# Performance work log

Hardware: AMD Instinct MI355X
Metric: run time of the kernel (lower is better)

The kernel has to match this reference:

```python
import jax, jax.numpy as jnp
import numpy as np

NUM_NODES = 15000


def _gcn_conv(x, W, b, src, dst, norm, num_nodes):
    # PyG GCNConv: x' = D^-1/2 (A + I) D^-1/2 (x W) + b
    h = x @ W                                   # [N, out]
    msg = h[src] * norm[:, None]                # gather + scale per edge
    out = jax.ops.segment_sum(msg, dst, num_segments=num_nodes)
    return out + b


def setup_inputs() -> dict:
    key = jax.random.key(0)
    ks = jax.random.split(key, 12)
    T = 100000
    E = 200000
    inp = {
        "x": jax.random.normal(ks[0], (NUM_NODES, 768), jnp.float32),
        "r_emb": jax.random.normal(ks[1], (T, 768), jnp.float32),
        "W1": jax.random.normal(ks[2], (768, 10), jnp.float32) * 0.05,
        "b1": jax.random.normal(ks[3], (10,), jnp.float32) * 0.05,
        "W2": jax.random.normal(ks[4], (10, 128), jnp.float32) * 0.05,
        "b2": jax.random.normal(ks[5], (128,), jnp.float32) * 0.05,
        "W_ih": jax.random.normal(ks[6], (512, 1024), jnp.float32) * 0.03,
        "W_hh": jax.random.normal(ks[7], (512, 128), jnp.float32) * 0.03,
        "b_ih": jax.random.normal(ks[8], (512,), jnp.float32) * 0.03,
        "b_hh": jax.random.normal(ks[9], (512,), jnp.float32) * 0.03,
        "edge_index": jax.random.randint(ks[10], (2, E), 0, NUM_NODES).astype(jnp.int64),
        "triples": jax.random.randint(ks[11], (T, 3), 0, NUM_NODES).astype(jnp.int64),
    }
    return inp


def reference(x, r_emb, W1, b1, W2, b2, W_ih, W_hh, b_ih, b_hh, edge_index, triples):
    N = x.shape[0]
    H = 128  # lstm hidden size
    # --- add self loops, symmetric GCN normalization ---
    loop = jnp.arange(N, dtype=edge_index.dtype)
    src = jnp.concatenate([edge_index[0], loop])
    dst = jnp.concatenate([edge_index[1], loop])
    deg = jax.ops.segment_sum(jnp.ones_like(dst, jnp.float32), dst, num_segments=N)
    dinv = jnp.where(deg > 0, jax.lax.rsqrt(deg), 0.0)
    norm = dinv[src] * dinv[dst]                      # [E+N]
    # --- 2-layer GCN ---
    h = jax.nn.relu(_gcn_conv(x, W1, b1, src, dst, norm, N))   # [N, 10]
    z = _gcn_conv(h, W2, b2, src, dst, norm, N)                # [N, 128]
    # --- per-triple LSTM scoring, batched (seq_len=1, zero init state) ---
    hvec = z[triples[:, 0]]                           # [T, 128]
    tvec = z[triples[:, 2]]                           # [T, 128]
    feat = jnp.concatenate([hvec, r_emb, tvec], axis=-1)       # [T, 1024]
    gates = feat @ W_ih.T + (b_ih + b_hh)             # [T, 512]; h0=0 so W_hh term vanishes
    i_g, f_g, g_g, o_g = jnp.split(gates, 4, axis=-1)  # torch gate order i,f,g,o
    c = jax.nn.sigmoid(i_g) * jnp.tanh(g_g)           # c0 = 0 -> forget term drops
    out = jax.nn.sigmoid(o_g) * jnp.tanh(c)           # [T, 128]
    score = jax.nn.sigmoid(jnp.sum(out, axis=-1))     # [T]
    return score
```

## Files before the change

### kernel.cpp

```cpp
#include <hip/hip_runtime.h>

#define NF 768
#define D1 10
#define D2 128
#define BM 64

typedef __attribute__((ext_vector_type(8))) short bf16x8;
typedef __attribute__((ext_vector_type(16))) float f32x16;

static __device__ __forceinline__ float sigf(float v){ return 1.0f/(1.0f+__expf(-v)); }
static __device__ __forceinline__ float tanhfast(float v){ return 2.0f/(1.0f+__expf(-2.0f*v)) - 1.0f; }
static __device__ __forceinline__ short f2bf(float f){
    unsigned u = __float_as_uint(f);
    u += 0x7fffu + ((u>>16)&1u);
    return (short)(u>>16);
}

static __device__ __forceinline__ void gload16(const void* g, void* l){
    __builtin_amdgcn_global_load_lds(
        (const __attribute__((address_space(1))) unsigned int*)(unsigned long long)g,
        (__attribute__((address_space(3))) unsigned int*)(unsigned long long)l,
        16, 0, 0);
}

static __device__ __forceinline__ bf16x8 cvt8(float4 a, float4 b){
    unsigned u0,u1,u2,u3;
    asm("v_cvt_pk_bf16_f32 %0, %1, %2" : "=v"(u0) : "v"(a.x), "v"(a.y));
    asm("v_cvt_pk_bf16_f32 %0, %1, %2" : "=v"(u1) : "v"(a.z), "v"(a.w));
    asm("v_cvt_pk_bf16_f32 %0, %1, %2" : "=v"(u2) : "v"(b.x), "v"(b.y));
    asm("v_cvt_pk_bf16_f32 %0, %1, %2" : "=v"(u3) : "v"(b.z), "v"(b.w));
    union { unsigned u[4]; bf16x8 v; } r;
    r.u[0]=u0; r.u[1]=u1; r.u[2]=u2; r.u[3]=u3;
    return r.v;
}

__global__ void k_deg(const int* __restrict__ dst, int* __restrict__ cnt, int E){
    int e = blockIdx.x*256 + threadIdx.x;
    if(e<E) atomicAdd(&cnt[dst[e]], 1);
}

__global__ __launch_bounds__(256) void k_scan(const int* __restrict__ cnt,
                                              int* __restrict__ rowptr, int* __restrict__ rowcur,
                                              float* __restrict__ dinv, int N, int E){
    __shared__ int part[256];
    int t = threadIdx.x;
    int C = (N+255)/256;
    int lo = t*C, hi = lo+C; if(hi>N) hi=N; if(lo>N) lo=N;
    int s=0;
    for(int i=lo;i<hi;i++) s += cnt[i];
    part[t]=s;
    __syncthreads();
    if(t==0){
        int run=0;
        for(int i=0;i<256;i++){ int v=part[i]; part[i]=run; run+=v; }
        rowptr[N]=E;
    }
    __syncthreads();
    int run = part[t];
    for(int i=lo;i<hi;i++){
        rowptr[i]=run; rowcur[i]=run; run += cnt[i];
        dinv[i] = rsqrtf((float)cnt[i] + 1.0f);
    }
}

__global__ void k_fill(const int* __restrict__ src, const int* __restrict__ dst,
                       const float* __restrict__ dinv, int* __restrict__ rowcur,
                       int* __restrict__ esrc, float* __restrict__ enorm, int E){
    int e = blockIdx.x*256 + threadIdx.x;
    if(e>=E) return;
    int s=src[e], d=dst[e];
    int pos = atomicAdd(&rowcur[d], 1);
    esrc[pos]=s;
    enorm[pos]=dinv[s]*dinv[d];
}

__global__ __launch_bounds__(256) void k_h1(const float* __restrict__ x,
                                            const float* __restrict__ W1,
                                            float* __restrict__ h1, int N){
    __shared__ float wt[D1*NF];
    for(int idx=threadIdx.x; idx<NF*D1; idx+=256){
        int k=idx/D1, c=idx-k*D1;
        wt[c*NF+k]=W1[idx];
    }
    __syncthreads();
    int row = blockIdx.x*4 + (threadIdx.x>>6);
    int lane = threadIdx.x&63;
    if(row>=N) return;
    const float4* xr = (const float4*)(x + (size_t)row*NF);
    float acc[D1];
#pragma unroll
    for(int c=0;c<D1;c++) acc[c]=0.f;
#pragma unroll
    for(int i=0;i<3;i++){
        float4 v = xr[lane + 64*i];
#pragma unroll
        for(int c=0;c<D1;c++){
            float4 w = *(const float4*)&wt[c*NF + (lane+64*i)*4];
            acc[c] += v.x*w.x + v.y*w.y + v.z*w.z + v.w*w.w;
        }
    }
#pragma unroll
    for(int c=0;c<D1;c++){
        float v=acc[c];
#pragma unroll
        for(int off=32;off;off>>=1) v += __shfl_down(v,off,64);
        acc[c]=v;
    }
    if(lane==0){
#pragma unroll
        for(int c=0;c<D1;c++) h1[(size_t)row*D1+c]=acc[c];
    }
}

__global__ __launch_bounds__(256) void k_gath1(const float* __restrict__ h1,
        const int* __restrict__ rowptr, const int* __restrict__ esrc,
        const float* __restrict__ enorm, const float* __restrict__ dinv,
        const float* __restrict__ b1, float* __restrict__ h, int N){
    int node = blockIdx.x*4 + (threadIdx.x>>6);
    int lane = threadIdx.x&63;
    if(node>=N) return;
    int e0=rowptr[node], e1=rowptr[node+1];
    float acc[D1];
#pragma unroll
    for(int c=0;c<D1;c++) acc[c]=0.f;
    for(int e=e0+lane; e<e1; e+=64){
        int s=esrc[e]; float w=enorm[e];
        const float* hr = h1 + (size_t)s*D1;
#pragma unroll
        for(int c=0;c<D1;c++) acc[c] += hr[c]*w;
    }
    if(lane==0){
        float di=dinv[node], d2=di*di;
        const float* hr = h1 + (size_t)node*D1;
#pragma unroll
        for(int c=0;c<D1;c++) acc[c] += hr[c]*d2;
    }
#pragma unroll
    for(int c=0;c<D1;c++){
        float v=acc[c];
#pragma unroll
        for(int off=32;off;off>>=1) v += __shfl_down(v,off,64);
        acc[c]=v;
    }
    if(lane==0){
#pragma unroll
        for(int c=0;c<D1;c++){
            float v = acc[c] + b1[c];
            h[(size_t)node*D1+c] = v>0.f ? v : 0.f;
        }
    }
}

__global__ __launch_bounds__(128) void k_hz(const float* __restrict__ h,
                                            const float* __restrict__ W2,
                                            float* __restrict__ hz, int N){
    __shared__ float w2s[D1*D2];
    int j = threadIdx.x;
    for(int i=j;i<D1*D2;i+=128) w2s[i]=W2[i];
    __syncthreads();
    int n = blockIdx.x;
    if(n>=N) return;
    const float* hr = h + (size_t)n*D1;
    float acc=0.f;
#pragma unroll
    for(int k=0;k<D1;k++) acc += hr[k]*w2s[k*D2+j];
    hz[(size_t)n*D2+j]=acc;
}

__global__ __launch_bounds__(128) void k_gath2(const float* __restrict__ hz,
        const int* __restrict__ rowptr, const int* __restrict__ esrc,
        const float* __restrict__ enorm, const float* __restrict__ dinv,
        const float* __restrict__ b2, float* __restrict__ zbf, int N){
    int n = blockIdx.x;
    int c = threadIdx.x;
    int e0 = rowptr[n], e1 = rowptr[n+1];
    float di = dinv[n];
    float acc = hz[(size_t)n*D2+c]*di*di + b2[c];
    int e = e0;
    for(; e+1<e1; e+=2){
        int s0=esrc[e], s1=esrc[e+1];
        float w0=enorm[e], w1=enorm[e+1];
        acc += hz[(size_t)s0*D2+c]*w0 + hz[(size_t)s1*D2+c]*w1;
    }
    if(e<e1) acc += hz[(size_t)esrc[e]*D2+c]*enorm[e];
    zbf[(size_t)n*D2+c] = acc;
}

__global__ void k_wimgB(const float* __restrict__ Wih, ushort* __restrict__ img){
    int gid = blockIdx.x*256 + threadIdx.x;
    if(gid >= 12*64*64) return;
    int l = gid & 63;
    int ks16 = (gid>>6) & 63;
    int f = gid >> 12;
    int dd = l & 31, kb = l>>5;
    int wn = f/3, gi = f - wn*3;
    int gbase = (gi==0)?0:((gi==1)?256:384);
    int wrow = gbase + wn*32 + dd;
    int k = ks16*16 + kb*8;
    const float* p = Wih + (size_t)wrow*1024 + k;
    float4 v0=*(const float4*)p, v1=*(const float4*)(p+4);
    bf16x8 o;
    o[0]=f2bf(v0.x); o[1]=f2bf(v0.y); o[2]=f2bf(v0.z); o[3]=f2bf(v0.w);
    o[4]=f2bf(v1.x); o[5]=f2bf(v1.y); o[6]=f2bf(v1.z); o[7]=f2bf(v1.w);
    *(bf16x8*)(img + (size_t)gid*8) = o;
}

__global__ __launch_bounds__(256,2) void k_big(
    const float* __restrict__ remb, const ushort* __restrict__ img,
    const float* __restrict__ zbf, const float* __restrict__ b_ih,
    const float* __restrict__ b_hh, const int* __restrict__ trip,
    float* __restrict__ score, int T)
{
    __shared__ float  Ar[4][64*32];
    __shared__ ushort Br[2][24*64*8];
    int tid=threadIdx.x, lane=tid&63, w=tid>>6;
    int l31=lane&31, lh=lane>>5;
    int t0=blockIdx.x*BM;

    const int arow = lane>>3;
    const int lsl  = ((lane&7) ^ arow)*4;
    int tcA[2], thA[2], ttA[2];
#pragma unroll
    for(int j=0;j<2;j++){
        int row = w*16 + j*8 + arow;
        int tc = t0+row; if(tc>=T) tc=T-1;
        tcA[j]=tc; thA[j]=trip[3*tc]; ttA[j]=trip[3*tc+2];
    }
    const int rx = l31&7;

    f32x16 acc[2][3];
    const f32x16 zer = {0,0,0,0,0,0,0,0,0,0,0,0,0,0,0,0};
#pragma unroll
    for(int m=0;m<2;m++)
#pragma unroll
        for(int g=0;g<3;g++) acc[m][g]=zer;

#define AISSUE(C_) if((C_)<32){ \
    _Pragma("unroll") \
    for(int j_=0;j_<2;j_++){ \
        const float* s_; \
        if((C_)<4)       s_ = zbf + (size_t)thA[j_]*D2 + (C_)*32 + lsl; \
        else if((C_)<28) s_ = remb + (size_t)tcA[j_]*NF + ((C_)-4)*32 + lsl; \
        else             s_ = zbf + (size_t)ttA[j_]*D2 + ((C_)-28)*32 + lsl; \
        gload16(s_, &Ar[(C_)&3][(w*16 + j_*8)*32]); \
    } }

#define BISSUE(C_) if((C_)<32){ \
    _Pragma("unroll") \
    for(int j_=0;j_<6;j_++){ \
        const int i_ = w*6+j_, f_ = i_>>1, s_ = i_&1; \
        gload16(img + ((size_t)(f_*64 + (C_)*2 + s_)*64 + lane)*8, \
                &Br[(C_)&1][(f_*2+s_)*64*8]); \
    } }

#define KSTEP(C_,S_) { \
    const float* ar_ = &Ar[(C_)&3][0]; \
    const ushort* br_ = &Br[(C_)&1][0]; \
    const int q0_ = (S_)*4 + lh*2; \
    float4 a00_ = *(const float4*)&ar_[ l31*32      + ((q0_  )^rx)*4 ]; \
    float4 a01_ = *(const float4*)&ar_[ l31*32      + ((q0_+1)^rx)*4 ]; \
    bf16x8 A0_ = cvt8(a00_,a01_); \
    float4 a10_ = *(const float4*)&ar_[ (32+l31)*32 + ((q0_  )^rx)*4 ]; \
    float4 a11_ = *(const float4*)&ar_[ (32+l31)*32 + ((q0_+1)^rx)*4 ]; \
    bf16x8 A1_ = cvt8(a10_,a11_); \
    bf16x8 B0_ = *(const bf16x8*)&br_[(((w*3+0)*2+(S_))*64 + lane)*8]; \
    bf16x8 B1_ = *(const bf16x8*)&br_[(((w*3+1)*2+(S_))*64 + lane)*8]; \
    bf16x8 B2_ = *(const bf16x8*)&br_[(((w*3+2)*2+(S_))*64 + lane)*8]; \
    acc[0][0]=__builtin_amdgcn_mfma_f32_32x32x16_bf16(A0_,B0_,acc[0][0],0,0,0); \
    acc[0][1]=__builtin_amdgcn_mfma_f32_32x32x16_bf16(A0_,B1_,acc[0][1],0,0,0); \
    acc[0][2]=__builtin_amdgcn_mfma_f32_32x32x16_bf16(A0_,B2_,acc[0][2],0,0,0); \
    acc[1][0]=__builtin_amdgcn_mfma_f32_32x32x16_bf16(A1_,B0_,acc[1][0],0,0,0); \
    acc[1][1]=__builtin_amdgcn_mfma_f32_32x32x16_bf16(A1_,B1_,acc[1][1],0,0,0); \
    acc[1][2]=__builtin_amdgcn_mfma_f32_32x32x16_bf16(A1_,B2_,acc[1][2],0,0,0); \
}

#define CHUNK(C_,W_) { \
    asm volatile("s_waitcnt vmcnt(" W_ ")" ::: "memory"); \
    __builtin_amdgcn_s_barrier(); \
    __builtin_amdgcn_sched_barrier(0); \
    BISSUE((C_)+1) \
    AISSUE((C_)+3) \
    __builtin_amdgcn_sched_barrier(0); \
    __builtin_amdgcn_s_setprio(1); \
    KSTEP(C_,0) KSTEP(C_,1) \
    __builtin_amdgcn_s_setprio(0); \
}

    AISSUE(0) AISSUE(1) BISSUE(0) AISSUE(2)
    __builtin_amdgcn_sched_barrier(0);

    CHUNK(0 ,"2") CHUNK(1 ,"2") CHUNK(2 ,"2") CHUNK(3 ,"2")
    CHUNK(4 ,"2") CHUNK(5 ,"2") CHUNK(6 ,"2") CHUNK(7 ,"2")
    CHUNK(8 ,"2") CHUNK(9 ,"2") CHUNK(10,"2") CHUNK(11,"2")
    CHUNK(12,"2") CHUNK(13,"2") CHUNK(14,"2") CHUNK(15,"2")
    CHUNK(16,"2") CHUNK(17,"2") CHUNK(18,"2") CHUNK(19,"2")
    CHUNK(20,"2") CHUNK(21,"2") CHUNK(22,"2") CHUNK(23,"2")
    CHUNK(24,"2") CHUNK(25,"2") CHUNK(26,"2") CHUNK(27,"2")
    CHUNK(28,"2") CHUNK(29,"2") CHUNK(30,"0") CHUNK(31,"0")
#undef CHUNK
#undef KSTEP
#undef BISSUE
#undef AISSUE

    float* rowsum = &Ar[0][0];
    __syncthreads();
    if(tid<BM) rowsum[tid]=0.f;
    __syncthreads();
    int d = w*32+l31;
    float bi=b_ih[d]+b_hh[d];
    float bg=b_ih[256+d]+b_hh[256+d];
    float bo=b_ih[384+d]+b_hh[384+d];
#pragma unroll
    for(int m=0;m<2;m++){
#pragma unroll
        for(int r=0;r<16;r++){
            int row = m*32 + (r&3)+8*(r>>2)+4*lh;
            float ig = acc[m][0][r] + bi;
            float gg = acc[m][1][r] + bg;
            float og = acc[m][2][r] + bo;
            float cc = sigf(ig)*tanhfast(gg);
            float ov = sigf(og)*tanhfast(cc);
#pragma unroll
            for(int off=1; off<32; off<<=1) ov += __shfl_xor(ov, off, 64);
            if(l31==0) atomicAdd(&rowsum[row], ov);
        }
    }
    __syncthreads();
    if(tid < BM){
        int t = t0 + tid;
        if(t < T) score[t] = sigf(rowsum[tid]);
    }
}

extern "C" void kernel_launch(void* const* d_in, const int* in_sizes, int n_in,
                              void* d_out, int out_size, void* d_ws, size_t ws_size,
                              hipStream_t stream){
    const float* x    = (const float*)d_in[0];
    const float* remb = (const float*)d_in[1];
    const float* W1   = (const float*)d_in[2];
    const float* b1   = (const float*)d_in[3];
    const float* W2   = (const float*)d_in[4];
    const float* b2   = (const float*)d_in[5];
    const float* Wih  = (const float*)d_in[6];
    const float* b_ih = (const float*)d_in[8];
    const float* b_hh = (const float*)d_in[9];
    const int*   ei   = (const int*)d_in[10];
    const int*   trip = (const int*)d_in[11];
    float* score = (float*)d_out;

    const int N = in_sizes[0]/NF;
    const int E = in_sizes[10]/2;
    const int T = in_sizes[11]/3;
    const int* src = ei;
    const int* dst = ei + E;

    float* ws = (float*)d_ws;
    size_t o = 0;
    ushort* img  = (ushort*)(ws+o); o += (size_t)12*64*64*8/2;
    float* zbf   = ws+o;            o += (size_t)N*D2;
    int*   cnt    = (int*)(ws+o);   o += (size_t)((N+8)&~7);
    int*   rowptr = (int*)(ws+o);   o += (size_t)((N+8)&~7);
    int*   rowcur = (int*)(ws+o);   o += (size_t)((N+8)&~7);
    int*   esrc   = (int*)(ws+o);   o += (size_t)E;
    float* enorm  = ws+o;           o += (size_t)E;
    float* dinv   = ws+o;           o += (size_t)((N+7)&~7);
    float* h1     = ws+o;           o += (size_t)N*D1;
    float* hbuf   = ws+o;           o += (size_t)N*D1;
    float* hz     = ws+o;           o += (size_t)N*D2;
    (void)ws_size; (void)n_in; (void)out_size;

    hipMemsetAsync(cnt, 0, (size_t)N*sizeof(int), stream);

    k_wimgB<<<dim3((12*64*64+255)/256), dim3(256), 0, stream>>>(Wih, img);
    k_deg  <<<dim3((E+255)/256), dim3(256), 0, stream>>>(dst, cnt, E);
    k_scan <<<dim3(1), dim3(256), 0, stream>>>(cnt, rowptr, rowcur, dinv, N, E);
    k_fill <<<dim3((E+255)/256), dim3(256), 0, stream>>>(src, dst, dinv, rowcur, esrc, enorm, E);
    k_h1   <<<dim3((N+3)/4), dim3(256), 0, stream>>>(x, W1, h1, N);
    k_gath1<<<dim3((N+3)/4), dim3(256), 0, stream>>>(h1, rowptr, esrc, enorm, dinv, b1, hbuf, N);
    k_hz   <<<dim3(N), dim3(128), 0, stream>>>(hbuf, W2, hz, N);
    k_gath2<<<dim3(N), dim3(128), 0, stream>>>(hz, rowptr, esrc, enorm, dinv, b2, zbf, N);
    k_big  <<<dim3((T+BM-1)/BM), dim3(256), 0, stream>>>(remb, img, zbf, b_ih, b_hh, trip, score, T);
}
```

Before: 324.5 us.

## Stage A operand as bf16 in LDS via register prefetch, triple-buffer B

The A operand (gathered z rows and r_emb) no longer goes through direct global-to-LDS copies as fp32. Each thread now loads it into registers, converts it to bf16 once, and writes a smaller swizzled bf16 tile to LDS. The K loop moves to 64 steps of 16, with B triple-buffered and a four-deep register prefetch of A, and the occupancy hint rises to 3 blocks per CU. This cuts LDS footprint and removes the redundant per-wave conversion, at the cost of more barriers per K element, more register pressure and exposure to register-load latency.

Result: faster. 302.2 us (-6.9%).

```diff
diff --git a/kernel.cpp b/kernel.cpp
--- a/kernel.cpp
+++ b/kernel.cpp
@@ -23,15 +23,13 @@
         16, 0, 0);
 }
 
-static __device__ __forceinline__ bf16x8 cvt8(float4 a, float4 b){
-    unsigned u0,u1,u2,u3;
+static __device__ __forceinline__ short4 cvt4(float4 a){
+    unsigned u0,u1;
     asm("v_cvt_pk_bf16_f32 %0, %1, %2" : "=v"(u0) : "v"(a.x), "v"(a.y));
     asm("v_cvt_pk_bf16_f32 %0, %1, %2" : "=v"(u1) : "v"(a.z), "v"(a.w));
-    asm("v_cvt_pk_bf16_f32 %0, %1, %2" : "=v"(u2) : "v"(b.x), "v"(b.y));
-    asm("v_cvt_pk_bf16_f32 %0, %1, %2" : "=v"(u3) : "v"(b.z), "v"(b.w));
-    union { unsigned u[4]; bf16x8 v; } r;
-    r.u[0]=u0; r.u[1]=u1; r.u[2]=u2; r.u[3]=u3;
-    return r.v;
+    union { unsigned u[2]; short4 s; } r;
+    r.u[0]=u0; r.u[1]=u1;
+    return r.s;
 }
 
 __global__ void k_deg(const int* __restrict__ dst, int* __restrict__ cnt, int E){
@@ -205,28 +203,28 @@
     *(bf16x8*)(img + (size_t)gid*8) = o;
 }
 
-__global__ __launch_bounds__(256,2) void k_big(
+__global__ __launch_bounds__(256,3) void k_big(
     const float* __restrict__ remb, const ushort* __restrict__ img,
     const float* __restrict__ zbf, const float* __restrict__ b_ih,
     const float* __restrict__ b_hh, const int* __restrict__ trip,
     float* __restrict__ score, int T)
 {
-    __shared__ float  Ar[4][64*32];
-    __shared__ ushort Br[2][24*64*8];
+    __shared__ ushort Ab[2][64*16];
+    __shared__ ushort Br[3][12*512];
     int tid=threadIdx.x, lane=tid&63, w=tid>>6;
     int l31=lane&31, lh=lane>>5;
     int t0=blockIdx.x*BM;
 
-    const int arow = lane>>3;
-    const int lsl  = ((lane&7) ^ arow)*4;
-    int tcA[2], thA[2], ttA[2];
-#pragma unroll
-    for(int j=0;j<2;j++){
-        int row = w*16 + j*8 + arow;
-        int tc = t0+row; if(tc>=T) tc=T-1;
-        tcA[j]=tc; thA[j]=trip[3*tc]; ttA[j]=trip[3*tc+2];
-    }
-    const int rx = l31&7;
+    const int arow = w*16 + (lane>>2);
+    const int asub = lane&3;
+    { }
+    int tc = t0 + arow; if(tc>=T) tc=T-1;
+    const float* pzh = zbf + (size_t)trip[3*tc]*D2   + asub*4;
+    const float* prm = remb + (size_t)tc*NF          + asub*4;
+    const float* pzt = zbf + (size_t)trip[3*tc+2]*D2 + asub*4;
+    const int awoff = arow*16 + (((asub>>1) ^ (arow&1))*8) + (asub&1)*4;
+    const int ar0 = (l31)*16    + ((lh ^ (l31&1))*8);
+    const int ar1 = (32+l31)*16 + ((lh ^ (l31&1))*8);
 
     f32x16 acc[2][3];
     const f32x16 zer = {0,0,0,0,0,0,0,0,0,0,0,0,0,0,0,0};
@@ -235,74 +233,75 @@
 #pragma unroll
         for(int g=0;g<3;g++) acc[m][g]=zer;
 
-#define AISSUE(C_) if((C_)<32){ \
+    float4 pa[4];
+
+#define ALOAD(C_) if((C_)<64){ \
+    const float* s_; \
+    if((C_)<8)       s_ = pzh + (C_)*16; \
+    else if((C_)<56) s_ = prm + ((C_)-8)*16; \
+    else             s_ = pzt + ((C_)-56)*16; \
+    pa[(C_)&3] = *(const float4*)s_; }
+
+#define AWRITE(C_) if((C_)<64){ \
+    *(short4*)&Ab[(C_)&1][awoff] = cvt4(pa[(C_)&3]); }
+
+#define BISSUE(C_) if((C_)<64){ \
     _Pragma("unroll") \
-    for(int j_=0;j_<2;j_++){ \
-        const float* s_; \
-        if((C_)<4)       s_ = zbf + (size_t)thA[j_]*D2 + (C_)*32 + lsl; \
-        else if((C_)<28) s_ = remb + (size_t)tcA[j_]*NF + ((C_)-4)*32 + lsl; \
-        else             s_ = zbf + (size_t)ttA[j_]*D2 + ((C_)-28)*32 + lsl; \
-        gload16(s_, &Ar[(C_)&3][(w*16 + j_*8)*32]); \
+    for(int j_=0;j_<3;j_++){ \
+        gload16(img + ((size_t)((w*3+j_)*64 + (C_))*64 + lane)*8, \
+                &Br[(C_)%3][(w*3+j_)*512]); \
     } }
 
-#define BISSUE(C_) if((C_)<32){ \
-    _Pragma("unroll") \
-    for(int j_=0;j_<6;j_++){ \
-        const int i_ = w*6+j_, f_ = i_>>1, s_ = i_&1; \
-        gload16(img + ((size_t)(f_*64 + (C_)*2 + s_)*64 + lane)*8, \
-                &Br[(C_)&1][(f_*2+s_)*64*8]); \
-    } }
-
-#define KSTEP(C_,S_) { \
-    const float* ar_ = &Ar[(C_)&3][0]; \
-    const ushort* br_ = &Br[(C_)&1][0]; \
-    const int q0_ = (S_)*4 + lh*2; \
-    float4 a00_ = *(const float4*)&ar_[ l31*32      + ((q0_  )^rx)*4 ]; \
-    float4 a01_ = *(const float4*)&ar_[ l31*32      + ((q0_+1)^rx)*4 ]; \
-    bf16x8 A0_ = cvt8(a00_,a01_); \
-    float4 a10_ = *(const float4*)&ar_[ (32+l31)*32 + ((q0_  )^rx)*4 ]; \
-    float4 a11_ = *(const float4*)&ar_[ (32+l31)*32 + ((q0_+1)^rx)*4 ]; \
-    bf16x8 A1_ = cvt8(a10_,a11_); \
-    bf16x8 B0_ = *(const bf16x8*)&br_[(((w*3+0)*2+(S_))*64 + lane)*8]; \
-    bf16x8 B1_ = *(const bf16x8*)&br_[(((w*3+1)*2+(S_))*64 + lane)*8]; \
-    bf16x8 B2_ = *(const bf16x8*)&br_[(((w*3+2)*2+(S_))*64 + lane)*8]; \
-    acc[0][0]=__builtin_amdgcn_mfma_f32_32x32x16_bf16(A0_,B0_,acc[0][0],0,0,0); \
-    acc[0][1]=__builtin_amdgcn_mfma_f32_32x32x16_bf16(A0_,B1_,acc[0][1],0,0,0); \
-    acc[0][2]=__builtin_amdgcn_mfma_f32_32x32x16_bf16(A0_,B2_,acc[0][2],0,0,0); \
-    acc[1][0]=__builtin_amdgcn_mfma_f32_32x32x16_bf16(A1_,B0_,acc[1][0],0,0,0); \
-    acc[1][1]=__builtin_amdgcn_mfma_f32_32x32x16_bf16(A1_,B1_,acc[1][1],0,0,0); \
-    acc[1][2]=__builtin_amdgcn_mfma_f32_32x32x16_bf16(A1_,B2_,acc[1][2],0,0,0); \
-}
-
-#define CHUNK(C_,W_) { \
+#define CH(C_,W_) { \
     asm volatile("s_waitcnt vmcnt(" W_ ")" ::: "memory"); \
+    __builtin_amdgcn_sched_barrier(0); \
+    asm volatile("s_waitcnt lgkmcnt(0)" ::: "memory"); \
     __builtin_amdgcn_s_barrier(); \
     __builtin_amdgcn_sched_barrier(0); \
-    BISSUE((C_)+1) \
-    AISSUE((C_)+3) \
+    BISSUE((C_)+2) \
     __builtin_amdgcn_sched_barrier(0); \
-    __builtin_amdgcn_s_setprio(1); \
-    KSTEP(C_,0) KSTEP(C_,1) \
-    __builtin_amdgcn_s_setprio(0); \
-}
-
-    AISSUE(0) AISSUE(1) BISSUE(0) AISSUE(2)
+    ALOAD((C_)+4) \
+    __builtin_amdgcn_sched_barrier(0); \
+    { \
+        const ushort* a_ = &Ab[(C_)&1][0]; \
+        const ushort* b_ = &Br[(C_)%3][0]; \
+        bf16x8 A0_ = *(const bf16x8*)&a_[ar0]; \
+        bf16x8 A1_ = *(const bf16x8*)&a_[ar1]; \
+        bf16x8 B0_ = *(const bf16x8*)&b_[((w*3+0)*64+lane)*8]; \
+        bf16x8 B1_ = *(const bf16x8*)&b_[((w*3+1)*64+lane)*8]; \
+        bf16x8 B2_ = *(const bf16x8*)&b_[((w*3+2)*64+lane)*8]; \
+        __builtin_amdgcn_s_setprio(1); \
+        acc[0][0]=__builtin_amdgcn_mfma_f32_32x32x16_bf16(A0_,B0_,acc[0][0],0,0,0); \
+        acc[0][1]=__builtin_amdgcn_mfma_f32_32x32x16_bf16(A0_,B1_,acc[0][1],0,0,0); \
+        acc[0][2]=__builtin_amdgcn_mfma_f32_32x32x16_bf16(A0_,B2_,acc[0][2],0,0,0); \
+        acc[1][0]=__builtin_amdgcn_mfma_f32_32x32x16_bf16(A1_,B0_,acc[1][0],0,0,0); \
+        acc[1][1]=__builtin_amdgcn_mfma_f32_32x32x16_bf16(A1_,B1_,acc[1][1],0,0,0); \
+        acc[1][2]=__builtin_amdgcn_mfma_f32_32x32x16_bf16(A1_,B2_,acc[1][2],0,0,0); \
+        __builtin_amdgcn_s_setprio(0); \
+    } \
+    AWRITE((C_)+1) \
+}
+
+    ALOAD(0) ALOAD(1) ALOAD(2) ALOAD(3)
     __builtin_amdgcn_sched_barrier(0);
-
-    CHUNK(0 ,"2") CHUNK(1 ,"2") CHUNK(2 ,"2") CHUNK(3 ,"2")
-    CHUNK(4 ,"2") CHUNK(5 ,"2") CHUNK(6 ,"2") CHUNK(7 ,"2")
-    CHUNK(8 ,"2") CHUNK(9 ,"2") CHUNK(10,"2") CHUNK(11,"2")
-    CHUNK(12,"2") CHUNK(13,"2") CHUNK(14,"2") CHUNK(15,"2")
-    CHUNK(16,"2") CHUNK(17,"2") CHUNK(18,"2") CHUNK(19,"2")
-    CHUNK(20,"2") CHUNK(21,"2") CHUNK(22,"2") CHUNK(23,"2")
-    CHUNK(24,"2") CHUNK(25,"2") CHUNK(26,"2") CHUNK(27,"2")
-    CHUNK(28,"2") CHUNK(29,"2") CHUNK(30,"0") CHUNK(31,"0")
-#undef CHUNK
-#undef KSTEP
+    BISSUE(0) BISSUE(1)
+    __builtin_amdgcn_sched_barrier(0);
+    AWRITE(0)
+
+    CH(0 ,"3") CH(1 ,"4") CH(2 ,"5") CH(3 ,"5") CH(4 ,"5") CH(5 ,"5") CH(6 ,"5") CH(7 ,"5")
+    CH(8 ,"5") CH(9 ,"5") CH(10,"5") CH(11,"5") CH(12,"5") CH(13,"5") CH(14,"5") CH(15,"5")
+    CH(16,"5") CH(17,"5") CH(18,"5") CH(19,"5") CH(20,"5") CH(21,"5") CH(22,"5") CH(23,"5")
+    CH(24,"5") CH(25,"5") CH(26,"5") CH(27,"5") CH(28,"5") CH(29,"5") CH(30,"5") CH(31,"5")
+    CH(32,"5") CH(33,"5") CH(34,"5") CH(35,"5") CH(36,"5") CH(37,"5") CH(38,"5") CH(39,"5")
+    CH(40,"5") CH(41,"5") CH(42,"5") CH(43,"5") CH(44,"5") CH(45,"5") CH(46,"5") CH(47,"5")
+    CH(48,"5") CH(49,"5") CH(50,"5") CH(51,"5") CH(52,"5") CH(53,"5") CH(54,"5") CH(55,"5")
+    CH(56,"5") CH(57,"5") CH(58,"5") CH(59,"5") CH(60,"5") CH(61,"4") CH(62,"3") CH(63,"0")
+#undef CH
 #undef BISSUE
-#undef AISSUE
-
-    float* rowsum = &Ar[0][0];
+#undef AWRITE
+#undef ALOAD
+
+    float* rowsum = (float*)&Br[0][0];
     __syncthreads();
     if(tid<BM) rowsum[tid]=0.f;
     __syncthreads();
```

## Replace multi-stage async LDS pipeline with single-buffered loop and raise occupancy

Applied to the files above, without the earlier changes.

Drops the 4-stage A and 2-stage B LDS ring buffers and the explicit vmcnt/sched_barrier pipeline, using one buffer per operand with two __syncthreads per k-chunk. Launch bounds go from 2 to 3 blocks per CU, relying on the smaller LDS footprint and more resident blocks to hide load latency instead of prefetching in software. The cost is exposed global-load latency inside each block and more barriers, and register pressure may be squeezed by the higher occupancy target.

After: 327.1 us. About the same (+0.8%).

```diff
diff --git a/kernel.cpp b/kernel.cpp
--- a/kernel.cpp
+++ b/kernel.cpp
@@ -205,28 +205,30 @@
     *(bf16x8*)(img + (size_t)gid*8) = o;
 }
 
-__global__ __launch_bounds__(256,2) void k_big(
+__global__ __launch_bounds__(256,3) void k_big(
     const float* __restrict__ remb, const ushort* __restrict__ img,
     const float* __restrict__ zbf, const float* __restrict__ b_ih,
     const float* __restrict__ b_hh, const int* __restrict__ trip,
     float* __restrict__ score, int T)
 {
-    __shared__ float  Ar[4][64*32];
-    __shared__ ushort Br[2][24*64*8];
+    __shared__ float  As[64*32];
+    __shared__ ushort Bs[24*64*8];
     int tid=threadIdx.x, lane=tid&63, w=tid>>6;
     int l31=lane&31, lh=lane>>5;
     int t0=blockIdx.x*BM;
 
-    const int arow = lane>>3;
-    const int lsl  = ((lane&7) ^ arow)*4;
-    int tcA[2], thA[2], ttA[2];
+    const int aoff = ((lane&7) ^ (lane>>3))*4;
+    const float* pzh[2]; const float* prm[2]; const float* pzt[2];
 #pragma unroll
     for(int j=0;j<2;j++){
-        int row = w*16 + j*8 + arow;
+        int row = w*16 + j*8 + (lane>>3);
         int tc = t0+row; if(tc>=T) tc=T-1;
-        tcA[j]=tc; thA[j]=trip[3*tc]; ttA[j]=trip[3*tc+2];
-    }
-    const int rx = l31&7;
+        pzh[j] = zbf + (size_t)trip[3*tc]*D2   + aoff;
+        prm[j] = remb + (size_t)tc*NF          + aoff;
+        pzt[j] = zbf + (size_t)trip[3*tc+2]*D2 + aoff;
+    }
+    float* adst0 = &As[(w*16+0)*32];
+    float* adst1 = &As[(w*16+8)*32];
 
     f32x16 acc[2][3];
     const f32x16 zer = {0,0,0,0,0,0,0,0,0,0,0,0,0,0,0,0};
@@ -235,75 +237,45 @@
 #pragma unroll
         for(int g=0;g<3;g++) acc[m][g]=zer;
 
-#define AISSUE(C_) if((C_)<32){ \
-    _Pragma("unroll") \
-    for(int j_=0;j_<2;j_++){ \
-        const float* s_; \
-        if((C_)<4)       s_ = zbf + (size_t)thA[j_]*D2 + (C_)*32 + lsl; \
-        else if((C_)<28) s_ = remb + (size_t)tcA[j_]*NF + ((C_)-4)*32 + lsl; \
-        else             s_ = zbf + (size_t)ttA[j_]*D2 + ((C_)-28)*32 + lsl; \
-        gload16(s_, &Ar[(C_)&3][(w*16 + j_*8)*32]); \
-    } }
-
-#define BISSUE(C_) if((C_)<32){ \
-    _Pragma("unroll") \
-    for(int j_=0;j_<6;j_++){ \
-        const int i_ = w*6+j_, f_ = i_>>1, s_ = i_&1; \
-        gload16(img + ((size_t)(f_*64 + (C_)*2 + s_)*64 + lane)*8, \
-                &Br[(C_)&1][(f_*2+s_)*64*8]); \
-    } }
-
-#define KSTEP(C_,S_) { \
-    const float* ar_ = &Ar[(C_)&3][0]; \
-    const ushort* br_ = &Br[(C_)&1][0]; \
-    const int q0_ = (S_)*4 + lh*2; \
-    float4 a00_ = *(const float4*)&ar_[ l31*32      + ((q0_  )^rx)*4 ]; \
-    float4 a01_ = *(const float4*)&ar_[ l31*32      + ((q0_+1)^rx)*4 ]; \
-    bf16x8 A0_ = cvt8(a00_,a01_); \
-    float4 a10_ = *(const float4*)&ar_[ (32+l31)*32 + ((q0_  )^rx)*4 ]; \
-    float4 a11_ = *(const float4*)&ar_[ (32+l31)*32 + ((q0_+1)^rx)*4 ]; \
-    bf16x8 A1_ = cvt8(a10_,a11_); \
-    bf16x8 B0_ = *(const bf16x8*)&br_[(((w*3+0)*2+(S_))*64 + lane)*8]; \
-    bf16x8 B1_ = *(const bf16x8*)&br_[(((w*3+1)*2+(S_))*64 + lane)*8]; \
-    bf16x8 B2_ = *(const bf16x8*)&br_[(((w*3+2)*2+(S_))*64 + lane)*8]; \
-    acc[0][0]=__builtin_amdgcn_mfma_f32_32x32x16_bf16(A0_,B0_,acc[0][0],0,0,0); \
-    acc[0][1]=__builtin_amdgcn_mfma_f32_32x32x16_bf16(A0_,B1_,acc[0][1],0,0,0); \
-    acc[0][2]=__builtin_amdgcn_mfma_f32_32x32x16_bf16(A0_,B2_,acc[0][2],0,0,0); \
-    acc[1][0]=__builtin_amdgcn_mfma_f32_32x32x16_bf16(A1_,B0_,acc[1][0],0,0,0); \
-    acc[1][1]=__builtin_amdgcn_mfma_f32_32x32x16_bf16(A1_,B1_,acc[1][1],0,0,0); \
-    acc[1][2]=__builtin_amdgcn_mfma_f32_32x32x16_bf16(A1_,B2_,acc[1][2],0,0,0); \
-}
-
-#define CHUNK(C_,W_) { \
-    asm volatile("s_waitcnt vmcnt(" W_ ")" ::: "memory"); \
-    __builtin_amdgcn_s_barrier(); \
-    __builtin_amdgcn_sched_barrier(0); \
-    BISSUE((C_)+1) \
-    AISSUE((C_)+3) \
-    __builtin_amdgcn_sched_barrier(0); \
-    __builtin_amdgcn_s_setprio(1); \
-    KSTEP(C_,0) KSTEP(C_,1) \
-    __builtin_amdgcn_s_setprio(0); \
-}
-
-    AISSUE(0) AISSUE(1) BISSUE(0) AISSUE(2)
-    __builtin_amdgcn_sched_barrier(0);
-
-    CHUNK(0 ,"2") CHUNK(1 ,"2") CHUNK(2 ,"2") CHUNK(3 ,"2")
-    CHUNK(4 ,"2") CHUNK(5 ,"2") CHUNK(6 ,"2") CHUNK(7 ,"2")
-    CHUNK(8 ,"2") CHUNK(9 ,"2") CHUNK(10,"2") CHUNK(11,"2")
-    CHUNK(12,"2") CHUNK(13,"2") CHUNK(14,"2") CHUNK(15,"2")
-    CHUNK(16,"2") CHUNK(17,"2") CHUNK(18,"2") CHUNK(19,"2")
-    CHUNK(20,"2") CHUNK(21,"2") CHUNK(22,"2") CHUNK(23,"2")
-    CHUNK(24,"2") CHUNK(25,"2") CHUNK(26,"2") CHUNK(27,"2")
-    CHUNK(28,"2") CHUNK(29,"2") CHUNK(30,"0") CHUNK(31,"0")
-#undef CHUNK
-#undef KSTEP
-#undef BISSUE
-#undef AISSUE
-
-    float* rowsum = &Ar[0][0];
-    __syncthreads();
+    const int rx7 = l31&7;
+
+    for(int s=0;s<32;s++){
+        const float *sa0, *sa1;
+        if(s<4)      { sa0=pzh[0]+s*32;      sa1=pzh[1]+s*32; }
+        else if(s<28){ sa0=prm[0]+(s-4)*32;  sa1=prm[1]+(s-4)*32; }
+        else         { sa0=pzt[0]+(s-28)*32; sa1=pzt[1]+(s-28)*32; }
+        gload16(sa0, adst0);
+        gload16(sa1, adst1);
+#pragma unroll
+        for(int j=0;j<6;j++){
+            int f = w*3 + (j>>1), sh = j&1;
+            gload16(img + ((size_t)(f*64 + s*2 + sh)*64 + lane)*8,
+                    &Bs[(size_t)((f*2+sh)*64)*8]);
+        }
+        __syncthreads();
+#pragma unroll
+        for(int h=0;h<2;h++){
+            int u0 = h*4 + lh*2;
+            float4 a00 = *(const float4*)&As[ l31*32     + ((u0  )^rx7)*4];
+            float4 a01 = *(const float4*)&As[ l31*32     + ((u0+1)^rx7)*4];
+            bf16x8 A0 = cvt8(a00,a01);
+            float4 a10 = *(const float4*)&As[(32+l31)*32 + ((u0  )^rx7)*4];
+            float4 a11 = *(const float4*)&As[(32+l31)*32 + ((u0+1)^rx7)*4];
+            bf16x8 A1 = cvt8(a10,a11);
+            bf16x8 B0 = *(const bf16x8*)&Bs[(size_t)(((w*3+0)*2+h)*64+lane)*8];
+            bf16x8 B1 = *(const bf16x8*)&Bs[(size_t)(((w*3+1)*2+h)*64+lane)*8];
+            bf16x8 B2 = *(const bf16x8*)&Bs[(size_t)(((w*3+2)*2+h)*64+lane)*8];
+            acc[0][0]=__builtin_amdgcn_mfma_f32_32x32x16_bf16(A0,B0,acc[0][0],0,0,0);
+            acc[0][1]=__builtin_amdgcn_mfma_f32_32x32x16_bf16(A0,B1,acc[0][1],0,0,0);
+            acc[0][2]=__builtin_amdgcn_mfma_f32_32x32x16_bf16(A0,B2,acc[0][2],0,0,0);
+            acc[1][0]=__builtin_amdgcn_mfma_f32_32x32x16_bf16(A1,B0,acc[1][0],0,0,0);
+            acc[1][1]=__builtin_amdgcn_mfma_f32_32x32x16_bf16(A1,B1,acc[1][1],0,0,0);
+            acc[1][2]=__builtin_amdgcn_mfma_f32_32x32x16_bf16(A1,B2,acc[1][2],0,0,0);
+        }
+        __syncthreads();
+    }
+
+    float* rowsum = &As[0];
     if(tid<BM) rowsum[tid]=0.f;
     __syncthreads();
     int d = w*32+l31;
```
